# Kernel tuning notes

Measured on AMD Instinct MI355X. Metric: run time of the kernel, lower is better.

## Reference

```python
import jax, jax.numpy as jnp
import numpy as np

B, S, D, F, E = 8, 2048, 512, 2048, 8


def setup_inputs() -> dict:
    key = jax.random.key(0)
    ks = jax.random.split(key, 7)
    x = jax.random.normal(ks[0], (B, S, D), dtype=jnp.float32)
    Wr = jax.random.normal(ks[1], (D, E), dtype=jnp.float32) * 0.02
    br = jnp.zeros((E,), dtype=jnp.float32)
    W1 = jax.random.normal(ks[2], (E, D, F), dtype=jnp.float32) * 0.02
    b1 = jnp.zeros((E, F), dtype=jnp.float32)
    W2 = jax.random.normal(ks[3], (E, F, D), dtype=jnp.float32) * 0.02
    b2 = jnp.zeros((E, D), dtype=jnp.float32)
    return {"x": x, "Wr": Wr, "br": br, "W1": W1, "b1": b1, "W2": W2, "b2": b2}


def reference(x, Wr, br, W1, b1, W2, b2):
    # Router: softmax gate + top-2
    logits = jnp.einsum('bsd,de->bse', x, Wr) + br            # [B,S,E]
    gate = jax.nn.softmax(logits, axis=-1)                    # [B,S,E]
    top2_val, top2_idx = jax.lax.top_k(gate, 2)               # [B,S,2]

    # Combine weights: gate value on the two selected experts, 0 elsewhere
    onehot = jax.nn.one_hot(top2_idx, E, dtype=x.dtype)       # [B,S,2,E]
    combine = jnp.sum(onehot * top2_val[..., None], axis=2)   # [B,S,E]

    # Dense per-expert FFN, masked-combined (same math as the token loop)
    out = jnp.zeros_like(x)
    for e in range(E):
        h = jax.nn.relu(jnp.einsum('bsd,df->bsf', x, W1[e]) + b1[e])
        y = jnp.einsum('bsf,fd->bsd', h, W2[e]) + b2[e]
        out = out + combine[..., e, None] * y

    # GShard-style load-balancing aux loss
    expert_prob = gate.mean(axis=(0, 1))                      # [E]
    aux_loss = jnp.sum(expert_prob * jnp.log(expert_prob + 1e-9))
    return out, aux_loss
```

## Files before the change

kernel.cpp:

```cpp
#include <hip/hip_runtime.h>
#include <math.h>

typedef unsigned short u16;
typedef __attribute__((ext_vector_type(8))) short short8;
typedef __attribute__((ext_vector_type(8))) u16 u16x8;
typedef __attribute__((ext_vector_type(4))) float f32x4;

#define NTOK 16384
#define DDIM 512
#define FDIM 2048
#define ENUM 8
#define NBLK 1024
#define APAD (32768 + 256)
#define MAXT 144

__device__ __forceinline__ u16 f2bf(float f) {
  unsigned u = __float_as_uint(f);
  u += 0x7FFFu + ((u >> 16) & 1u);
  return (u16)(u >> 16);
}
__device__ __forceinline__ float bf2f(u16 b) {
  return __uint_as_float(((unsigned)b) << 16);
}

typedef const __attribute__((address_space(1))) unsigned int* gas1_t;
typedef __attribute__((address_space(3))) unsigned int* las3_t;
__device__ __forceinline__ void gload16(const u16* g, u16* l) {
  __builtin_amdgcn_global_load_lds((gas1_t)(const void*)g, (las3_t)(void*)l, 16, 0, 0);
}

__global__ __launch_bounds__(256) void router_kernel(
    const float* __restrict__ x, const float* __restrict__ Wr,
    const float* __restrict__ br, int* __restrict__ top2e,
    float* __restrict__ top2v, int* __restrict__ histBase,
    float* __restrict__ gatePart) {
  __shared__ __align__(16) float sWr[DDIM * ENUM];
  __shared__ __align__(16) float sX[4][DDIM];
  __shared__ int sHist[ENUM];
  __shared__ float sGate[ENUM];
  int tid = threadIdx.x;
  for (int i = tid; i < DDIM * ENUM; i += 256) sWr[i] = Wr[i];
  if (tid < ENUM) { sHist[tid] = 0; sGate[tid] = 0.f; }
  __syncthreads();
  int wave = tid >> 6, lane = tid & 63;
  int e = lane >> 3, dg = lane & 7;
  float bre = br[e];
  for (int it = 0; it < 4; ++it) {
    int t = blockIdx.x * 16 + wave * 4 + it;
    const float4* xr = (const float4*)(x + (size_t)t * DDIM);
    float4* sx4 = (float4*)sX[wave];
    sx4[lane] = xr[lane];
    sx4[lane + 64] = xr[lane + 64];
    asm volatile("s_waitcnt lgkmcnt(0)" ::: "memory");
    float acc = 0.f;
#pragma unroll 16
    for (int i = 0; i < 64; ++i) {
      float xv = sX[wave][i * 8 + dg];
      acc += xv * sWr[(i * 8 + dg) * 8 + e];
    }
    acc += __shfl_xor(acc, 1);
    acc += __shfl_xor(acc, 2);
    acc += __shfl_xor(acc, 4);
    float logit = acc + bre;
    float m = logit;
    m = fmaxf(m, __shfl_xor(m, 8));
    m = fmaxf(m, __shfl_xor(m, 16));
    m = fmaxf(m, __shfl_xor(m, 32));
    float pv = expf(logit - m);
    float s = pv;
    s += __shfl_xor(s, 8);
    s += __shfl_xor(s, 16);
    s += __shfl_xor(s, 32);
    float gate = pv / s;
    float v1 = gate; int i1 = e;
#pragma unroll
    for (int msk = 8; msk <= 32; msk <<= 1) {
      float ov = __shfl_xor(v1, msk);
      int oi = __shfl_xor(i1, msk);
      if (ov > v1 || (ov == v1 && oi < i1)) { v1 = ov; i1 = oi; }
    }
    float g2 = (e == i1) ? -1.f : gate;
    float v2 = g2; int i2 = e;
#pragma unroll
    for (int msk = 8; msk <= 32; msk <<= 1) {
      float ov = __shfl_xor(v2, msk);
      int oi = __shfl_xor(i2, msk);
      if (ov > v2 || (ov == v2 && oi < i2)) { v2 = ov; i2 = oi; }
    }
    if (lane == 0) {
      top2e[2 * t] = i1; top2e[2 * t + 1] = i2;
      top2v[2 * t] = v1; top2v[2 * t + 1] = v2;
      atomicAdd(&sHist[i1], 1);
      atomicAdd(&sHist[i2], 1);
    }
    if (dg == 0) atomicAdd(&sGate[e], gate);
  }
  __syncthreads();
  if (tid < ENUM) {
    histBase[blockIdx.x * 8 + tid] = sHist[tid];
    gatePart[blockIdx.x * 8 + tid] = sGate[tid];
  }
}

__global__ __launch_bounds__(256) void scan_kernel(
    int* __restrict__ histBase, const float* __restrict__ gatePart,
    int* __restrict__ offsets, int* __restrict__ counts,
    int* __restrict__ tileE, int* __restrict__ tileM, int* __restrict__ nTiles,
    float* __restrict__ auxOut) {
  __shared__ int sTot[ENUM];
  __shared__ float sG[ENUM];
  int tid = threadIdx.x, wave = tid >> 6, lane = tid & 63;
  if (tid < ENUM) sG[tid] = 0.f;
  __syncthreads();
  float loc[8] = {0, 0, 0, 0, 0, 0, 0, 0};
  for (int r = tid; r < NBLK; r += 256) {
#pragma unroll
    for (int e = 0; e < 8; ++e) loc[e] += gatePart[r * 8 + e];
  }
#pragma unroll
  for (int e = 0; e < 8; ++e) atomicAdd(&sG[e], loc[e]);
#pragma unroll
  for (int ei = 0; ei < 2; ++ei) {
    int e = wave * 2 + ei;
    int running = 0;
    for (int itb = 0; itb < NBLK / 64; ++itb) {
      int idx = (itb * 64 + lane) * 8 + e;
      int v = histBase[idx];
      int inc = v;
#pragma unroll
      for (int d = 1; d < 64; d <<= 1) {
        int o = __shfl_up(inc, d);
        if (lane >= d) inc += o;
      }
      histBase[idx] = running + inc - v;
      running += __shfl(inc, 63);
    }
    if (lane == 0) sTot[e] = running;
  }
  __syncthreads();
  if (tid == 0) {
    int off = 0, nt = 0;
#pragma unroll
    for (int e = 0; e < 8; ++e) {
      int c = sTot[e];
      offsets[e] = off; counts[e] = c; off += c;
      int mt = (c + 255) >> 8;
      for (int m = 0; m < mt; ++m) { tileE[nt] = e; tileM[nt] = m; ++nt; }
    }
    *nTiles = nt;
    float aux = 0.f;
#pragma unroll
    for (int e = 0; e < 8; ++e) {
      float pr = sG[e] / (float)NTOK;
      aux += pr * logf(pr + 1e-9f);
    }
    *auxOut = aux;
  }
}

__global__ __launch_bounds__(256) void place_kernel(
    const float* __restrict__ x, const int* __restrict__ top2e,
    const float* __restrict__ top2v, const int* __restrict__ histBase,
    const int* __restrict__ offsets, int* __restrict__ tokA,
    float* __restrict__ assignW, u16* __restrict__ Xg) {
  __shared__ int sA[32];
  int tid = threadIdx.x, wave = tid >> 6, lane = tid & 63;
  int blk = blockIdx.x;
  if (tid < 32) {
    int slot = tid;
    int t = blk * 16 + (slot >> 1);
    int e = top2e[2 * t + (slot & 1)];
    float v = top2v[2 * t + (slot & 1)];
    int rank = 0;
#pragma unroll
    for (int ee = 0; ee < 8; ++ee) {
      unsigned long long mm = __ballot(e == ee);
      if (e == ee) rank = __popcll(mm & ((1ull << slot) - 1));
    }
    int a = offsets[e] + histBase[blk * 8 + e] + rank;
    sA[slot] = a;
    tokA[2 * t + (slot & 1)] = a;
    assignW[a] = v;
  }
  __syncthreads();
  for (int it = 0; it < 4; ++it) {
    int lt = wave * 4 + it;
    int t = blk * 16 + lt;
    const float4* xr = (const float4*)(x + (size_t)t * DDIM);
    float4 v0 = xr[lane * 2], v1 = xr[lane * 2 + 1];
    u16x8 o;
    o[0] = f2bf(v0.x); o[1] = f2bf(v0.y); o[2] = f2bf(v0.z); o[3] = f2bf(v0.w);
    o[4] = f2bf(v1.x); o[5] = f2bf(v1.y); o[6] = f2bf(v1.z); o[7] = f2bf(v1.w);
    int a1 = sA[2 * lt], a2 = sA[2 * lt + 1];
    *(u16x8*)(Xg + (size_t)a1 * DDIM + lane * 8) = o;
    *(u16x8*)(Xg + (size_t)a2 * DDIM + lane * 8) = o;
  }
}

__global__ __launch_bounds__(256) void transpose_kernel(
    const float* __restrict__ W, u16* __restrict__ WT, int K, int N) {
  __shared__ float tile[64][65];
  int e = blockIdx.y;
  int tn_count = N >> 6;
  int tk = blockIdx.x / tn_count;
  int tn = blockIdx.x - tk * tn_count;
  const float* Wp = W + (size_t)e * K * N;
  u16* WTp = WT + (size_t)e * N * K;
  int c = threadIdx.x & 63, r = threadIdx.x >> 6;
#pragma unroll
  for (int i = 0; i < 16; ++i) {
    int row = r + i * 4;
    tile[row][c] = Wp[(size_t)(tk * 64 + row) * N + tn * 64 + c];
  }
  __syncthreads();
#pragma unroll
  for (int i = 0; i < 16; ++i) {
    int row = r + i * 4;
    WTp[(size_t)(tn * 64 + row) * K + tk * 64 + c] = f2bf(tile[c][row]);
  }
}


#define STG(SP0, SP1, SOP, SBUF, SKH, SKT)                                     \
  do {                                                                         \
    const size_t go_ = (size_t)(SKT) * 64 + (SKH) * 32;                        \
    gload16((SP0) + go_, (u16*)(ldsB + (SOP) * 65536 + (SBUF) * 32768 +        \
                                (SKH) * 16384 + w1024));                       \
    gload16((SP1) + go_, (u16*)(ldsB + (SOP) * 65536 + (SBUF) * 32768 +        \
                                (SKH) * 16384 + 8192 + w1024));                \
  } while (0)

#define PH(MH, KS, CBUF, SP0, SP1, SOP, SBUF, SKH, SKT, GATE)                  \
  do {                                                                         \
    short8 areg[4];                                                            \
    _Pragma("unroll")                                                          \
    for (int m_ = 0; m_ < 4; ++m_)                                             \
      areg[m_] = *(const short8*)(ldsB + (CBUF) * 32768 + (KS) * 16384 +       \
                                  (MH) * 4096 + m_ * 1024 + frA);              \
    if ((MH) == 0) {                                                           \
      _Pragma("unroll")                                                        \
      for (int n_ = 0; n_ < 4; ++n_)                                           \
        breg[n_] = *(const short8*)(ldsB + 65536 + (CBUF) * 32768 +            \
                                    (KS) * 16384 + n_ * 1024 + frB);           \
    }                                                                          \
    STG(SP0, SP1, SOP, SBUF, SKH, SKT);                                        \
    if (GATE) asm volatile("s_waitcnt vmcnt(8)" ::: "memory");                 \
    __builtin_amdgcn_s_barrier();                                              \
    __builtin_amdgcn_sched_barrier(0);                                         \
    __builtin_amdgcn_s_setprio(1);                                             \
    _Pragma("unroll")                                                          \
    for (int m_ = 0; m_ < 4; ++m_)                                             \
      _Pragma("unroll")                                                        \
      for (int n_ = 0; n_ < 4; ++n_)                                           \
        acc[(MH) * 4 + m_][n_] = __builtin_amdgcn_mfma_f32_16x16x32_bf16(      \
            areg[m_], breg[n_], acc[(MH) * 4 + m_][n_], 0, 0, 0);              \
    __builtin_amdgcn_s_setprio(0);                                             \
    __builtin_amdgcn_s_barrier();                                              \
    __builtin_amdgcn_sched_barrier(0);                                         \
  } while (0)

template <int K>
__device__ __forceinline__ void mainloop8(const u16* __restrict__ A,
                                          const u16* __restrict__ B,
                                          char* ldsB, f32x4 (&acc)[8][4]) {
  const int tid = threadIdx.x;
  const int lane = tid & 63, wave = tid >> 6;
  const int wr = wave >> 2, wc = wave & 3;
  const int fr = lane & 15;
  const int swzRd = (((lane >> 4) ^ ((lane >> 1) & 3)) & 3) * 16;
  const int frA = (wr * 128 + fr) * 64 + swzRd;
  const int frB = (wc * 64 + fr) * 64 + swzRd;
  const int w1024 = wave * 1024;
  const int rowS = wave * 16 + (lane >> 2);
  const int cswz = ((lane & 3) ^ ((lane >> 3) & 3)) * 8;
  const u16* bA0 = A + (size_t)rowS * K + cswz;
  const u16* bA1 = A + (size_t)(rowS + 128) * K + cswz;
  const u16* bB0 = B + (size_t)rowS * K + cswz;
  const u16* bB1 = B + (size_t)(rowS + 128) * K + cswz;
  const int KT = K / 64, NIT = KT / 2;
  short8 breg[4];

  STG(bA0, bA1, 0, 0, 0, 0);
  STG(bB0, bB1, 1, 0, 0, 0);
  STG(bA0, bA1, 0, 0, 1, 0);
  STG(bB0, bB1, 1, 0, 1, 0);
  STG(bA0, bA1, 0, 1, 0, 1);
  STG(bB0, bB1, 1, 1, 0, 1);
  asm volatile("s_waitcnt vmcnt(8)" ::: "memory");
  __builtin_amdgcn_s_barrier();
  __builtin_amdgcn_sched_barrier(0);

#pragma unroll 1
  for (int it = 0; it < NIT; ++it) {
    const int t1 = 2 * it + 1;
    const int t2 = (2 * it + 2) & (KT - 1);
    const int t3 = (2 * it + 3) & (KT - 1);
    PH(0, 0, 0, bA0, bA1, 0, 1, 1, t1, 0);
    PH(1, 0, 0, bB0, bB1, 1, 1, 1, t1, 1);
    PH(0, 1, 0, bA0, bA1, 0, 0, 0, t2, 0);
    PH(1, 1, 0, bB0, bB1, 1, 0, 0, t2, 1);
    PH(0, 0, 1, bA0, bA1, 0, 0, 1, t2, 0);
    PH(1, 0, 1, bB0, bB1, 1, 0, 1, t2, 1);
    PH(0, 1, 1, bA0, bA1, 0, 1, 0, t3, 0);
    PH(1, 1, 1, bB0, bB1, 1, 1, 0, t3, 1);
  }
}

__global__ __launch_bounds__(512, 1) void gemm1_kernel(
    const u16* __restrict__ Xg, const u16* __restrict__ W1T,
    const float* __restrict__ b1, u16* __restrict__ h,
    const int* __restrict__ counts, const int* __restrict__ offsets,
    const int* __restrict__ tileE, const int* __restrict__ tileM,
    const int* __restrict__ nTiles) {
  extern __shared__ char ldsB[];
  if ((int)blockIdx.x >= *nTiles) return;
  int e = tileE[blockIdx.x], mtile = tileM[blockIdx.x];
  int ntile = blockIdx.y;
  int cnt = counts[e], off = offsets[e];
  const u16* A = Xg + (size_t)(off + mtile * 256) * DDIM;
  const u16* B = W1T + ((size_t)e * FDIM + ntile * 256) * DDIM;
  f32x4 acc[8][4] = {};
  mainloop8<DDIM>(A, B, ldsB, acc);
  int lane = threadIdx.x & 63, wave = threadIdx.x >> 6;
  int wr = wave >> 2, wc = wave & 3;
  int cl = lane & 15, rq = (lane >> 4) * 4;
#pragma unroll
  for (int ai = 0; ai < 8; ++ai) {
#pragma unroll
    for (int i = 0; i < 4; ++i) {
      int gr = mtile * 256 + wr * 128 + ai * 16 + rq + i;
      if (gr < cnt) {
#pragma unroll
        for (int n = 0; n < 4; ++n) {
          int gc = ntile * 256 + wc * 64 + n * 16 + cl;
          float v = acc[ai][n][i] + b1[e * FDIM + gc];
          v = fmaxf(v, 0.f);
          h[(size_t)(off + gr) * FDIM + gc] = f2bf(v);
        }
      }
    }
  }
}

__global__ __launch_bounds__(512, 1) void gemm2_kernel(
    const u16* __restrict__ h, const u16* __restrict__ W2T,
    const float* __restrict__ b2, const float* __restrict__ assignW,
    const int* __restrict__ counts, const int* __restrict__ offsets,
    const int* __restrict__ tileE, const int* __restrict__ tileM,
    const int* __restrict__ nTiles, u16* __restrict__ z) {
  extern __shared__ char ldsB[];
  if ((int)blockIdx.x >= *nTiles) return;
  int e = tileE[blockIdx.x], mtile = tileM[blockIdx.x];
  int ntile = blockIdx.y;
  int cnt = counts[e], off = offsets[e];
  const u16* A = h + (size_t)(off + mtile * 256) * FDIM;
  const u16* B = W2T + ((size_t)e * DDIM + ntile * 256) * FDIM;
  f32x4 acc[8][4] = {};
  mainloop8<FDIM>(A, B, ldsB, acc);
  int lane = threadIdx.x & 63, wave = threadIdx.x >> 6;
  int wr = wave >> 2, wc = wave & 3;
  int cl = lane & 15, rq = (lane >> 4) * 4;
#pragma unroll
  for (int ai = 0; ai < 8; ++ai) {
#pragma unroll
    for (int i = 0; i < 4; ++i) {
      int gr = mtile * 256 + wr * 128 + ai * 16 + rq + i;
      if (gr < cnt) {
        int a = off + gr;
        float w = assignW[a];
#pragma unroll
        for (int n = 0; n < 4; ++n) {
          int gc = ntile * 256 + wc * 64 + n * 16 + cl;
          float v = (acc[ai][n][i] + b2[e * DDIM + gc]) * w;
          z[(size_t)a * DDIM + gc] = f2bf(v);
        }
      }
    }
  }
}

__global__ __launch_bounds__(256) void combine_kernel(
    const u16* __restrict__ z, const int* __restrict__ tokA,
    float* __restrict__ out) {
  int tid = threadIdx.x, wave = tid >> 6, lane = tid & 63;
  int t = blockIdx.x * 4 + wave;
  int a1 = tokA[2 * t], a2 = tokA[2 * t + 1];
  u16x8 v1 = *(const u16x8*)(z + (size_t)a1 * DDIM + lane * 8);
  u16x8 v2 = *(const u16x8*)(z + (size_t)a2 * DDIM + lane * 8);
  float4 o0, o1;
  o0.x = bf2f(v1[0]) + bf2f(v2[0]);
  o0.y = bf2f(v1[1]) + bf2f(v2[1]);
  o0.z = bf2f(v1[2]) + bf2f(v2[2]);
  o0.w = bf2f(v1[3]) + bf2f(v2[3]);
  o1.x = bf2f(v1[4]) + bf2f(v2[4]);
  o1.y = bf2f(v1[5]) + bf2f(v2[5]);
  o1.z = bf2f(v1[6]) + bf2f(v2[6]);
  o1.w = bf2f(v1[7]) + bf2f(v2[7]);
  float4* o = (float4*)(out + (size_t)t * DDIM + lane * 8);
  o[0] = o0;
  o[1] = o1;
}

extern "C" void kernel_launch(void* const* d_in, const int* in_sizes, int n_in,
                              void* d_out, int out_size, void* d_ws, size_t ws_size,
                              hipStream_t stream) {
  const float* x  = (const float*)d_in[0];
  const float* Wr = (const float*)d_in[1];
  const float* br = (const float*)d_in[2];
  const float* W1 = (const float*)d_in[3];
  const float* b1 = (const float*)d_in[4];
  const float* W2 = (const float*)d_in[5];
  const float* b2 = (const float*)d_in[6];
  float* out = (float*)d_out;

  char* ws = (char*)d_ws;
  size_t p = 0;
  auto alloc = [&](size_t bytes) -> void* {
    void* r = ws + p;
    p = (p + bytes + 255) & ~(size_t)255;
    return r;
  };
  int* counts     = (int*)alloc(ENUM * 4);
  int* offsets    = (int*)alloc(ENUM * 4);
  int* nTiles     = (int*)alloc(4);
  int* tileE      = (int*)alloc(MAXT * 4);
  int* tileM      = (int*)alloc(MAXT * 4);
  int* top2e      = (int*)alloc((size_t)NTOK * 2 * 4);
  float* top2v    = (float*)alloc((size_t)NTOK * 2 * 4);
  int* tokA       = (int*)alloc((size_t)NTOK * 2 * 4);
  float* assignW  = (float*)alloc((size_t)APAD * 4);
  int* histBase   = (int*)alloc((size_t)NBLK * 8 * 4);
  float* gatePart = (float*)alloc((size_t)NBLK * 8 * 4);
  u16* W1T        = (u16*)alloc((size_t)ENUM * FDIM * DDIM * 2);
  u16* W2T        = (u16*)alloc((size_t)ENUM * DDIM * FDIM * 2);
  u16* Xg         = (u16*)alloc((size_t)APAD * DDIM * 2);
  u16* hbuf       = (u16*)alloc((size_t)APAD * FDIM * 2);
  u16* z          = Xg;
  (void)in_sizes; (void)n_in; (void)out_size; (void)ws_size;

  (void)hipFuncSetAttribute((const void*)gemm1_kernel,
                            hipFuncAttributeMaxDynamicSharedMemorySize, 131072);
  (void)hipFuncSetAttribute((const void*)gemm2_kernel,
                            hipFuncAttributeMaxDynamicSharedMemorySize, 131072);

  transpose_kernel<<<dim3(256, 8), 256, 0, stream>>>(W1, W1T, DDIM, FDIM);
  transpose_kernel<<<dim3(256, 8), 256, 0, stream>>>(W2, W2T, FDIM, DDIM);
  router_kernel<<<NBLK, 256, 0, stream>>>(x, Wr, br, top2e, top2v, histBase,
                                          gatePart);
  scan_kernel<<<1, 256, 0, stream>>>(histBase, gatePart, offsets, counts,
                                     tileE, tileM, nTiles,
                                     out + (size_t)NTOK * DDIM);
  place_kernel<<<NBLK, 256, 0, stream>>>(x, top2e, top2v, histBase, offsets,
                                         tokA, assignW, Xg);
  gemm1_kernel<<<dim3(MAXT, 8), 512, 131072, stream>>>(
      Xg, W1T, b1, hbuf, counts, offsets, tileE, tileM, nTiles);
  gemm2_kernel<<<dim3(MAXT, 2), 512, 131072, stream>>>(
      hbuf, W2T, b2, assignW, counts, offsets, tileE, tileM, nTiles, z);
  combine_kernel<<<NTOK / 4, 256, 0, stream>>>(z, tokA, out);
}
```

Before: 327.8 us.

## Use 128-row tiles for GEMM2, remap GEMM grids, and merge vectorized weight transposes

GEMM2 now uses a new 128x256 tile mainloop with 96KB LDS in place of the 256x256 tiles. This doubles the number of work tiles so more CUs are occupied for the K=2048 down-projection. Both GEMMs switch to a 1D grid with a remapped tile order so that neighbouring workgroups spread across XCDs. The two weight transposes are merged into a single launch with float4 loads and 16-byte bf16 stores. The smaller tile gives less operand reuse per block and raises the number of W2 reloads.

```diff
diff --git a/kernel.cpp b/kernel.cpp
--- a/kernel.cpp
+++ b/kernel.cpp
@@ -12,7 +12,10 @@
 #define ENUM 8
 #define NBLK 1024
 #define APAD (32768 + 256)
-#define MAXT 144
+#define NT1CAP 136
+#define NT2CAP 264
+#define G1GRID 1088
+#define G2GRID 528
 
 __device__ __forceinline__ u16 f2bf(float f) {
   unsigned u = __float_as_uint(f);
@@ -105,8 +108,9 @@
 __global__ __launch_bounds__(256) void scan_kernel(
     int* __restrict__ histBase, const float* __restrict__ gatePart,
     int* __restrict__ offsets, int* __restrict__ counts,
-    int* __restrict__ tileE, int* __restrict__ tileM, int* __restrict__ nTiles,
-    float* __restrict__ auxOut) {
+    int* __restrict__ tileE1, int* __restrict__ tileM1,
+    int* __restrict__ tileE2, int* __restrict__ tileM2,
+    int* __restrict__ nT, float* __restrict__ auxOut) {
   __shared__ int sTot[ENUM];
   __shared__ float sG[ENUM];
   int tid = threadIdx.x, wave = tid >> 6, lane = tid & 63;
@@ -139,15 +143,17 @@
   }
   __syncthreads();
   if (tid == 0) {
-    int off = 0, nt = 0;
+    int off = 0, nt1 = 0, nt2 = 0;
 #pragma unroll
     for (int e = 0; e < 8; ++e) {
       int c = sTot[e];
       offsets[e] = off; counts[e] = c; off += c;
-      int mt = (c + 255) >> 8;
-      for (int m = 0; m < mt; ++m) { tileE[nt] = e; tileM[nt] = m; ++nt; }
-    }
-    *nTiles = nt;
+      int mt1 = (c + 255) >> 8;
+      for (int m = 0; m < mt1; ++m) { tileE1[nt1] = e; tileM1[nt1] = m; ++nt1; }
+      int mt2 = (c + 127) >> 7;
+      for (int m = 0; m < mt2; ++m) { tileE2[nt2] = e; tileM2[nt2] = m; ++nt2; }
+    }
+    nT[0] = nt1; nT[1] = nt2;
     float aux = 0.f;
 #pragma unroll
     for (int e = 0; e < 8; ++e) {
@@ -198,28 +204,35 @@
 }
 
 __global__ __launch_bounds__(256) void transpose_kernel(
-    const float* __restrict__ W, u16* __restrict__ WT, int K, int N) {
+    const float* __restrict__ W1, const float* __restrict__ W2,
+    u16* __restrict__ W1T, u16* __restrict__ W2T) {
   __shared__ float tile[64][65];
-  int e = blockIdx.y;
-  int tn_count = N >> 6;
-  int tk = blockIdx.x / tn_count;
-  int tn = blockIdx.x - tk * tn_count;
-  const float* Wp = W + (size_t)e * K * N;
-  u16* WTp = WT + (size_t)e * N * K;
-  int c = threadIdx.x & 63, r = threadIdx.x >> 6;
-#pragma unroll
-  for (int i = 0; i < 16; ++i) {
-    int row = r + i * 4;
-    tile[row][c] = Wp[(size_t)(tk * 64 + row) * N + tn * 64 + c];
+  int q = threadIdx.x;
+  int half = blockIdx.y >> 3, e = blockIdx.y & 7;
+  const float* W = half ? W2 : W1;
+  u16* WT = half ? W2T : W1T;
+  int K = half ? FDIM : DDIM, N = half ? DDIM : FDIM;
+  int tnc = N >> 6;
+  int tk = blockIdx.x / tnc, tn = blockIdx.x - tk * tnc;
+  const float* Wp = W + (size_t)e * K * N + (size_t)(tk * 64) * N + tn * 64;
+#pragma unroll
+  for (int i = 0; i < 4; ++i) {
+    int row = (q >> 4) + i * 16, c4 = (q & 15) * 4;
+    float4 v = *(const float4*)(Wp + (size_t)row * N + c4);
+    tile[row][c4] = v.x; tile[row][c4 + 1] = v.y;
+    tile[row][c4 + 2] = v.z; tile[row][c4 + 3] = v.w;
   }
   __syncthreads();
-#pragma unroll
-  for (int i = 0; i < 16; ++i) {
-    int row = r + i * 4;
-    WTp[(size_t)(tn * 64 + row) * K + tk * 64 + c] = f2bf(tile[c][row]);
-  }
-}
-
+  u16* WTp = WT + (size_t)e * N * K + (size_t)(tn * 64) * K + tk * 64;
+#pragma unroll
+  for (int p = 0; p < 2; ++p) {
+    int n = (q >> 3) + p * 32, k0 = (q & 7) * 8;
+    u16x8 o;
+#pragma unroll
+    for (int j = 0; j < 8; ++j) o[j] = f2bf(tile[k0 + j][n]);
+    *(u16x8*)(WTp + (size_t)n * K + k0) = o;
+  }
+}
 
 #define STG(SP0, SP1, SOP, SBUF, SKH, SKT)                                     \
   do {                                                                         \
@@ -310,12 +323,14 @@
     const u16* __restrict__ Xg, const u16* __restrict__ W1T,
     const float* __restrict__ b1, u16* __restrict__ h,
     const int* __restrict__ counts, const int* __restrict__ offsets,
-    const int* __restrict__ tileE, const int* __restrict__ tileM,
-    const int* __restrict__ nTiles) {
+    const int* __restrict__ tileE1, const int* __restrict__ tileM1,
+    const int* __restrict__ nT) {
   extern __shared__ char ldsB[];
-  if ((int)blockIdx.x >= *nTiles) return;
-  int e = tileE[blockIdx.x], mtile = tileM[blockIdx.x];
-  int ntile = blockIdx.y;
+  int wg = blockIdx.x;
+  int L = (wg & 7) * (G1GRID / 8) + (wg >> 3);
+  int tile = L >> 3, ntile = L & 7;
+  if (tile >= nT[0]) return;
+  int e = tileE1[tile], mtile = tileM1[tile];
   int cnt = counts[e], off = offsets[e];
   const u16* A = Xg + (size_t)(off + mtile * 256) * DDIM;
   const u16* B = W1T + ((size_t)e * FDIM + ntile * 256) * DDIM;
@@ -342,36 +357,113 @@
   }
 }
 
+#define STG2(SBUF, SKH, SKT)                                                   \
+  do {                                                                         \
+    const size_t go_ = (size_t)(SKT) * 64 + (SKH) * 32;                        \
+    gload16(a2g + go_, (u16*)(ldsB + (SBUF) * 16384 + (SKH) * 8192 + w1024));  \
+    gload16(b2g0 + go_, (u16*)(ldsB + 32768 + (SBUF) * 32768 +                 \
+                               (SKH) * 16384 + w1024));                        \
+    gload16(b2g1 + go_, (u16*)(ldsB + 32768 + (SBUF) * 32768 +                 \
+                               (SKH) * 16384 + 8192 + w1024));                 \
+  } while (0)
+
+#define PH2(KS, CBUF, SBUF, SKH, SKT)                                          \
+  do {                                                                         \
+    short8 areg[4], breg2[4];                                                  \
+    _Pragma("unroll")                                                          \
+    for (int m_ = 0; m_ < 4; ++m_)                                             \
+      areg[m_] = *(const short8*)(ldsB + (CBUF) * 16384 + (KS) * 8192 +        \
+                                  m_ * 1024 + frA2);                           \
+    _Pragma("unroll")                                                          \
+    for (int n_ = 0; n_ < 4; ++n_)                                             \
+      breg2[n_] = *(const short8*)(ldsB + 32768 + (CBUF) * 32768 +             \
+                                   (KS) * 16384 + n_ * 1024 + frB2);           \
+    STG2(SBUF, SKH, SKT);                                                      \
+    asm volatile("s_waitcnt vmcnt(6)" ::: "memory");                           \
+    __builtin_amdgcn_s_barrier();                                              \
+    __builtin_amdgcn_sched_barrier(0);                                         \
+    __builtin_amdgcn_s_setprio(1);                                             \
+    _Pragma("unroll")                                                          \
+    for (int m_ = 0; m_ < 4; ++m_)                                             \
+      _Pragma("unroll")                                                        \
+      for (int n_ = 0; n_ < 4; ++n_)                                           \
+        acc[m_][n_] = __builtin_amdgcn_mfma_f32_16x16x32_bf16(                 \
+            areg[m_], breg2[n_], acc[m_][n_], 0, 0, 0);                        \
+    __builtin_amdgcn_s_setprio(0);                                             \
+    __builtin_amdgcn_s_barrier();                                              \
+    __builtin_amdgcn_sched_barrier(0);                                         \
+  } while (0)
+
+template <int K>
+__device__ __forceinline__ void mainloop2(const u16* __restrict__ A,
+                                          const u16* __restrict__ B,
+                                          char* ldsB, f32x4 (&acc)[4][4]) {
+  const int tid = threadIdx.x;
+  const int lane = tid & 63, wave = tid >> 6;
+  const int wr = wave >> 2, wc = wave & 3;
+  const int fr = lane & 15;
+  const int slot = ((lane >> 4) ^ ((lane >> 1) & 3)) & 3;
+  const int frA2 = (wr * 64 + fr) * 64 + slot * 16;
+  const int frB2 = (wc * 64 + fr) * 64 + slot * 16;
+  const int w1024 = wave * 1024;
+  const int rowS = tid >> 2;
+  const int cswz = ((tid & 3) ^ ((tid >> 3) & 3)) * 8;
+  const u16* a2g = A + (size_t)rowS * K + cswz;
+  const u16* b2g0 = B + (size_t)rowS * K + cswz;
+  const u16* b2g1 = B + (size_t)(rowS + 128) * K + cswz;
+  const int KT = K / 64;
+
+  STG2(0, 0, 0);
+  STG2(0, 1, 0);
+  STG2(1, 0, 1);
+  asm volatile("s_waitcnt vmcnt(6)" ::: "memory");
+  __builtin_amdgcn_s_barrier();
+  __builtin_amdgcn_sched_barrier(0);
+
+#pragma unroll 1
+  for (int tt = 0; tt < KT / 2; ++tt) {
+    const int t0 = 2 * tt;
+    const int u2 = (t0 + 2) & (KT - 1);
+    const int u3 = (t0 + 3) & (KT - 1);
+    PH2(0, 0, 1, 1, t0 + 1);
+    PH2(1, 0, 0, 0, u2);
+    PH2(0, 1, 0, 1, u2);
+    PH2(1, 1, 1, 0, u3);
+  }
+}
+
 __global__ __launch_bounds__(512, 1) void gemm2_kernel(
     const u16* __restrict__ h, const u16* __restrict__ W2T,
     const float* __restrict__ b2, const float* __restrict__ assignW,
     const int* __restrict__ counts, const int* __restrict__ offsets,
-    const int* __restrict__ tileE, const int* __restrict__ tileM,
-    const int* __restrict__ nTiles, u16* __restrict__ z) {
+    const int* __restrict__ tileE2, const int* __restrict__ tileM2,
+    const int* __restrict__ nT, u16* __restrict__ z) {
   extern __shared__ char ldsB[];
-  if ((int)blockIdx.x >= *nTiles) return;
-  int e = tileE[blockIdx.x], mtile = tileM[blockIdx.x];
-  int ntile = blockIdx.y;
+  int wg = blockIdx.x;
+  int L = (wg & 7) * (G2GRID / 8) + (wg >> 3);
+  int tile = L >> 1, ntile = L & 1;
+  if (tile >= nT[1]) return;
+  int e = tileE2[tile], mtile = tileM2[tile];
   int cnt = counts[e], off = offsets[e];
-  const u16* A = h + (size_t)(off + mtile * 256) * FDIM;
+  const u16* A = h + (size_t)(off + mtile * 128) * FDIM;
   const u16* B = W2T + ((size_t)e * DDIM + ntile * 256) * FDIM;
-  f32x4 acc[8][4] = {};
-  mainloop8<FDIM>(A, B, ldsB, acc);
+  f32x4 acc[4][4] = {};
+  mainloop2<FDIM>(A, B, ldsB, acc);
   int lane = threadIdx.x & 63, wave = threadIdx.x >> 6;
   int wr = wave >> 2, wc = wave & 3;
   int cl = lane & 15, rq = (lane >> 4) * 4;
 #pragma unroll
-  for (int ai = 0; ai < 8; ++ai) {
+  for (int m = 0; m < 4; ++m) {
 #pragma unroll
     for (int i = 0; i < 4; ++i) {
-      int gr = mtile * 256 + wr * 128 + ai * 16 + rq + i;
+      int gr = mtile * 128 + wr * 64 + m * 16 + rq + i;
       if (gr < cnt) {
         int a = off + gr;
         float w = assignW[a];
 #pragma unroll
         for (int n = 0; n < 4; ++n) {
           int gc = ntile * 256 + wc * 64 + n * 16 + cl;
-          float v = (acc[ai][n][i] + b2[e * DDIM + gc]) * w;
+          float v = (acc[m][n][i] + b2[e * DDIM + gc]) * w;
           z[(size_t)a * DDIM + gc] = f2bf(v);
         }
       }
@@ -422,9 +514,11 @@
   };
   int* counts     = (int*)alloc(ENUM * 4);
   int* offsets    = (int*)alloc(ENUM * 4);
-  int* nTiles     = (int*)alloc(4);
-  int* tileE      = (int*)alloc(MAXT * 4);
-  int* tileM      = (int*)alloc(MAXT * 4);
+  int* nT         = (int*)alloc(2 * 4);
+  int* tileE1     = (int*)alloc(NT1CAP * 4);
+  int* tileM1     = (int*)alloc(NT1CAP * 4);
+  int* tileE2     = (int*)alloc(NT2CAP * 4);
+  int* tileM2     = (int*)alloc(NT2CAP * 4);
   int* top2e      = (int*)alloc((size_t)NTOK * 2 * 4);
   float* top2v    = (float*)alloc((size_t)NTOK * 2 * 4);
   int* tokA       = (int*)alloc((size_t)NTOK * 2 * 4);
@@ -441,20 +535,19 @@
   (void)hipFuncSetAttribute((const void*)gemm1_kernel,
                             hipFuncAttributeMaxDynamicSharedMemorySize, 131072);
   (void)hipFuncSetAttribute((const void*)gemm2_kernel,
-                            hipFuncAttributeMaxDynamicSharedMemorySize, 131072);
-
-  transpose_kernel<<<dim3(256, 8), 256, 0, stream>>>(W1, W1T, DDIM, FDIM);
-  transpose_kernel<<<dim3(256, 8), 256, 0, stream>>>(W2, W2T, FDIM, DDIM);
+                            hipFuncAttributeMaxDynamicSharedMemorySize, 98304);
+
+  transpose_kernel<<<dim3(256, 16), 256, 0, stream>>>(W1, W2, W1T, W2T);
   router_kernel<<<NBLK, 256, 0, stream>>>(x, Wr, br, top2e, top2v, histBase,
                                           gatePart);
   scan_kernel<<<1, 256, 0, stream>>>(histBase, gatePart, offsets, counts,
-                                     tileE, tileM, nTiles,
+                                     tileE1, tileM1, tileE2, tileM2, nT,
                                      out + (size_t)NTOK * DDIM);
   place_kernel<<<NBLK, 256, 0, stream>>>(x, top2e, top2v, histBase, offsets,
                                          tokA, assignW, Xg);
-  gemm1_kernel<<<dim3(MAXT, 8), 512, 131072, stream>>>(
-      Xg, W1T, b1, hbuf, counts, offsets, tileE, tileM, nTiles);
-  gemm2_kernel<<<dim3(MAXT, 2), 512, 131072, stream>>>(
-      hbuf, W2T, b2, assignW, counts, offsets, tileE, tileM, nTiles, z);
+  gemm1_kernel<<<G1GRID, 512, 131072, stream>>>(
+      Xg, W1T, b1, hbuf, counts, offsets, tileE1, tileM1, nT);
+  gemm2_kernel<<<G2GRID, 512, 98304, stream>>>(
+      hbuf, W2T, b2, assignW, counts, offsets, tileE2, tileM2, nT, z);
   combine_kernel<<<NTOK / 4, 256, 0, stream>>>(z, tokA, out);
 }
```

Result: faster. 317.3 us (-3.2%).
